# Kernel tuning notes

Measured on AMD Instinct MI355X. Metric: run time of the kernel, lower is better.

The kernel has to match this reference:

```python
import jax, jax.numpy as jnp
import numpy as np
from jax.scipy.special import gammaln

N_NODES = 50000
N_EDGES = 500000
IN_DIM = 256
OUT_DIM = 128
NEG_SLOPE = 0.01  # F.leaky_relu default


def setup_inputs() -> dict:
    key = jax.random.key(0)
    kh, kw, ka, ks, kd, kdist = jax.random.split(key, 6)
    h = jax.random.normal(kh, (N_NODES, IN_DIM), dtype=jnp.float32)
    # xavier-normal-ish scale for the learned weights
    fc_w = jax.random.normal(kw, (OUT_DIM, IN_DIM), dtype=jnp.float32) * 0.05
    attn_w = jax.random.normal(ka, (1, 2 * OUT_DIM), dtype=jnp.float32) * 0.05
    src = jax.random.randint(ks, (N_EDGES,), 0, N_NODES, dtype=jnp.int32)
    dst = jax.random.randint(kd, (N_EDGES,), 0, N_NODES, dtype=jnp.int32)
    dist = jax.random.randint(kdist, (N_EDGES,), 0, 100, dtype=jnp.int32)
    return {"h": h, "fc_w": fc_w, "attn_w": attn_w, "src": src, "dst": dst, "dist": dist}


def _poisson_pmf(k, mu):
    # poisson.pmf(k, mu) = exp(k*log(mu) - mu - lgamma(k+1))
    return jnp.exp(k * jnp.log(mu) - mu - gammaln(k + 1.0))


def reference(h, fc_w, attn_w, src, dst, dist):
    # node transform: z = fc(h), [N, out]
    z = h @ fc_w.T
    zs = z[src]            # [E, out] gathered source feats
    zd = z[dst]            # [E, out] gathered dest feats
    # attn_fc(cat([z_src, z_dst])) split into two dots
    a = zs @ attn_w[0, :OUT_DIM] + zd @ attn_w[0, OUT_DIM:]   # [E]
    e = jnp.where(a >= 0, a, NEG_SLOPE * a)                    # leaky_relu
    # poisson weighting: k = dist // 2, mu = mean(dists)
    dist_f = dist.astype(jnp.float32)
    mu = jnp.mean(dist_f)
    k = jnp.floor(dist_f / 2.0)
    probs = _poisson_pmf(k, mu)
    e = probs * e                                              # [E]
    # segment softmax over incoming edges of each dst node
    m = jax.ops.segment_max(e, dst, num_segments=N_NODES)      # [N]
    ex = jnp.exp(e - m[dst])                                   # [E]
    denom = jax.ops.segment_sum(ex, dst, num_segments=N_NODES) # [N]
    alpha = ex / denom[dst]                                    # [E]
    # weighted scatter-sum of source feats
    h_out = jax.ops.segment_sum(alpha[:, None] * zs, dst, num_segments=N_NODES)
    return h_out
```

## Files before the change

### kernel.cpp

```cpp
#include <hip/hip_runtime.h>
#include <math.h>

#define N_NODES 50000
#define N_EDGES 500000
#define IN_DIM 256
#define OUT_DIM 128
#define NEG_SLOPE 0.01f
#define NB_ZERO 196
#define MAX_DEG 128

typedef __attribute__((ext_vector_type(8))) short short8;
typedef __attribute__((ext_vector_type(4))) float f32x4;

__device__ __forceinline__ unsigned short f2bf(float f) {
  unsigned u = __float_as_uint(f);
  unsigned r = (u + 0x7FFFu + ((u >> 16) & 1u)) >> 16;
  return (unsigned short)r;
}
__device__ __forceinline__ float bflo(unsigned u) {
  return __uint_as_float((u & 0xFFFFu) << 16);
}
__device__ __forceinline__ float bfhi(unsigned u) {
  return __uint_as_float(u & 0xFFFF0000u);
}

__global__ __launch_bounds__(256) void prep_kernel(
    const float* __restrict__ W, unsigned short* __restrict__ Wb,
    int* __restrict__ p) {
  const int i = blockIdx.x * 256 + threadIdx.x;
  if (i < N_NODES + 1) p[i] = 0;
  if (i < IN_DIM * OUT_DIM) Wb[i] = f2bf(W[i]);
}

__global__ __launch_bounds__(512, 4) void gemm_mfma_kernel(
    const float* __restrict__ h, const unsigned short* __restrict__ Wb,
    const float* __restrict__ aw,
    unsigned short* __restrict__ zb, float* __restrict__ s1, float* __restrict__ s2) {
  __shared__ unsigned short Blds[128 * 256];
  const int t    = threadIdx.x;
  const int wid  = t >> 6;
  const int lane = t & 63;
  const int row0 = blockIdx.x * 128 + wid * 16;
  const int r16  = lane & 15;
  const int kg   = lane >> 4;

#pragma unroll
  for (int it = 0; it < 8; ++it) {
    const int c   = it * 512 + t;
    const int row = c >> 5, kc = c & 31;
    *(float4*)&Blds[row * 256 + ((kc ^ (row & 7)) << 3)] =
        *(const float4*)&Wb[row * 256 + (kc << 3)];
  }

  const int arow = row0 + r16;
  const size_t hbase = (size_t)((arow < N_NODES) ? arow : (N_NODES - 1)) * IN_DIM;
  float4 a0[8], a1[8];
#pragma unroll
  for (int ks = 0; ks < 8; ++ks) {
    const int k0 = ks * 32 + kg * 8;
    a0[ks] = *(const float4*)&h[hbase + k0];
    a1[ks] = *(const float4*)&h[hbase + k0 + 4];
  }

  f32x4 acc[8];
#pragma unroll
  for (int ct = 0; ct < 8; ++ct) acc[ct] = (f32x4)(0.f);

  __syncthreads();

#pragma unroll
  for (int ks = 0; ks < 8; ++ks) {
    const int k0 = ks * 32 + kg * 8;
    short8 af;
    af[0] = (short)f2bf(a0[ks].x); af[1] = (short)f2bf(a0[ks].y);
    af[2] = (short)f2bf(a0[ks].z); af[3] = (short)f2bf(a0[ks].w);
    af[4] = (short)f2bf(a1[ks].x); af[5] = (short)f2bf(a1[ks].y);
    af[6] = (short)f2bf(a1[ks].z); af[7] = (short)f2bf(a1[ks].w);
#pragma unroll
    for (int ct = 0; ct < 8; ++ct) {
      const int brow = ct * 16 + r16;
      const short8 bf =
          *(const short8*)&Blds[brow * 256 + (k0 ^ ((r16 & 7) << 3))];
      acc[ct] = __builtin_amdgcn_mfma_f32_16x16x32_bf16(af, bf, acc[ct], 0, 0, 0);
    }
  }

#pragma unroll
  for (int q = 0; q < 4; ++q) {
    const int zr = row0 + kg * 4 + q;
    if (zr < N_NODES) {
#pragma unroll
      for (int ct = 0; ct < 8; ++ct)
        zb[(size_t)zr * OUT_DIM + ct * 16 + r16] = f2bf(acc[ct][q]);
    }
  }

  float p1[4] = {0.f, 0.f, 0.f, 0.f}, p2[4] = {0.f, 0.f, 0.f, 0.f};
#pragma unroll
  for (int ct = 0; ct < 8; ++ct) {
    const float w1 = aw[ct * 16 + r16];
    const float w2 = aw[128 + ct * 16 + r16];
#pragma unroll
    for (int q = 0; q < 4; ++q) {
      p1[q] += acc[ct][q] * w1;
      p2[q] += acc[ct][q] * w2;
    }
  }
#pragma unroll
  for (int off = 8; off; off >>= 1) {
#pragma unroll
    for (int q = 0; q < 4; ++q) {
      p1[q] += __shfl_xor(p1[q], off);
      p2[q] += __shfl_xor(p2[q], off);
    }
  }
  if (r16 == 0) {
#pragma unroll
    for (int q = 0; q < 4; ++q) {
      const int zr = row0 + kg * 4 + q;
      if (zr < N_NODES) { s1[zr] = p1[q]; s2[zr] = p2[q]; }
    }
  }
}

__global__ __launch_bounds__(256) void mean_hist_kernel(
    const int* __restrict__ dist, const int* __restrict__ dst,
    int* __restrict__ isum, int* __restrict__ cnt, int* __restrict__ rank) {
  int tid = blockIdx.x * blockDim.x + threadIdx.x;
  int stride = gridDim.x * blockDim.x;
  int acc = 0;
  for (int i = tid; i < N_EDGES; i += stride) {
    acc += dist[i];
    rank[i] = atomicAdd(&cnt[dst[i]], 1);
  }
#pragma unroll
  for (int off = 32; off; off >>= 1) acc += __shfl_down(acc, off);
  if ((threadIdx.x & 63) == 0) atomicAdd(isum, acc);
}

__global__ __launch_bounds__(128) void lut_kernel(
    const int* __restrict__ isum, float* __restrict__ lut) {
  const int d = threadIdx.x;
  if (d >= 100) return;
  const float mu = (float)(*isum) * (1.0f / N_EDGES);
  const float k = (float)(d >> 1);
  lut[d] = expf(k * logf(mu) - mu - lgammaf(k + 1.0f));
}

__global__ __launch_bounds__(256) void fill_kernel(
    const int* __restrict__ dst, const int* __restrict__ src,
    const int* __restrict__ dist, const int* __restrict__ rank,
    const float* __restrict__ s1, const float* __restrict__ s2,
    const float* __restrict__ lut, float2* __restrict__ epair) {
  int i = blockIdx.x * blockDim.x + threadIdx.x;
  if (i >= N_EDGES) return;
  const int d = dst[i];
  const int s = src[i];
  const int r = rank[i];
  if (r >= MAX_DEG) return;
  const float p = lut[dist[i]];
  const float a = s1[s] + s2[d];
  const float ev = p * ((a >= 0.f) ? a : NEG_SLOPE * a);
  epair[(size_t)d * MAX_DEG + r] = make_float2(expf(ev), __int_as_float(s));
}

__global__ __launch_bounds__(256) void node_kernel(
    const int* __restrict__ cnt, const float2* __restrict__ epair,
    const uint4* __restrict__ zb4, float* __restrict__ out) {
  const int wid = threadIdx.x >> 6, lane = threadIdx.x & 63;
  const int n = blockIdx.x * 4 + wid;
  if (n >= N_NODES) return;
  const size_t beg = (size_t)n * MAX_DEG;
  const int deg = min(cnt[n], MAX_DEG);

  const int q     = lane >> 4;
  const int laneQ = lane & 15;

  float acc[8] = {0.f, 0.f, 0.f, 0.f, 0.f, 0.f, 0.f, 0.f};
  if (deg > 0) {
    float ss = 0.f;
    for (int j = lane; j < deg; j += 64) ss += epair[beg + j].x;
#pragma unroll
    for (int off = 32; off; off >>= 1) ss += __shfl_xor(ss, off);
    const float inv = 1.0f / ss;

#pragma unroll 2
    for (int jj = 0; jj < deg; jj += 4) {
      int j2 = jj + q;
      const float w = (j2 < deg) ? 1.0f : 0.0f;
      j2 = (j2 < deg) ? j2 : jj;
      const float2 pr = epair[beg + j2];
      const float al = pr.x * inv * w;
      const int   sj = __float_as_int(pr.y);
      const uint4 v = zb4[(size_t)sj * 16 + laneQ];
      acc[0] += al * bflo(v.x); acc[1] += al * bfhi(v.x);
      acc[2] += al * bflo(v.y); acc[3] += al * bfhi(v.y);
      acc[4] += al * bflo(v.z); acc[5] += al * bfhi(v.z);
      acc[6] += al * bflo(v.w); acc[7] += al * bfhi(v.w);
    }
  }

#pragma unroll
  for (int k = 0; k < 8; ++k) {
    acc[k] += __shfl_down(acc[k], 16);
    acc[k] += __shfl_down(acc[k], 32);
  }
  if (lane < 16) {
    float* orow = &out[(size_t)n * OUT_DIM + laneQ * 8];
    *(float4*)&orow[0] = make_float4(acc[0], acc[1], acc[2], acc[3]);
    *(float4*)&orow[4] = make_float4(acc[4], acc[5], acc[6], acc[7]);
  }
}

extern "C" void kernel_launch(void* const* d_in, const int* in_sizes, int n_in,
                              void* d_out, int out_size, void* d_ws, size_t ws_size,
                              hipStream_t stream) {
  const float* h    = (const float*)d_in[0];
  const float* fc_w = (const float*)d_in[1];
  const float* attn = (const float*)d_in[2];
  const int*   src  = (const int*)d_in[3];
  const int*   dst  = (const int*)d_in[4];
  const int*   dist = (const int*)d_in[5];
  float* out = (float*)d_out;
  float* ws  = (float*)d_ws;

  unsigned short* zb    = (unsigned short*)ws;
  float*          s1    = ws + 3200000;
  float*          s2    = ws + 3250000;
  int*            cnt   = (int*)(ws + 3300000);
  int*            isum  = (int*)(ws + 3350000);
  float*          lut   = ws + 3350004;
  int*            rank  = (int*)(ws + 3350104);
  float2*         epair = (float2*)(ws + 3850104);
  unsigned short* Wb    = (unsigned short*)(ws + 16650104);

  prep_kernel<<<NB_ZERO, 256, 0, stream>>>(fc_w, Wb, cnt);
  gemm_mfma_kernel<<<(N_NODES + 127) / 128, 512, 0, stream>>>(h, Wb, attn, zb, s1, s2);
  mean_hist_kernel<<<256, 256, 0, stream>>>(dist, dst, isum, cnt, rank);
  lut_kernel<<<1, 128, 0, stream>>>(isum, lut);
  fill_kernel<<<(N_EDGES + 255) / 256, 256, 0, stream>>>(
      dst, src, dist, rank, s1, s2, lut, epair);
  node_kernel<<<(N_NODES + 3) / 4, 256, 0, stream>>>(
      cnt, epair, (const uint4*)zb, out);
}
```

Baseline: 94.83 us.

## Fuse edge scoring into node kernel and pack src/dist slots during histogram

The histogram kernel now writes each edge's src index and dist, packed into 32 bits, straight into its per-destination slot, which removes the rank array. The separate fill kernel is gone. The node kernel computes the leaky-relu attention, Poisson weight and exp per edge itself and stages weight/index pairs in shared memory. This cuts one launch and the 8-byte epair write and read, at the cost of random s1 reads inside the node kernel. The packing relies on src < 65536 and dist < 65536, and the grid uses N_NODES/4, which assumes N_NODES is divisible by 4.

```diff
diff --git a/kernel.cpp b/kernel.cpp
--- a/kernel.cpp
+++ b/kernel.cpp
@@ -125,13 +125,18 @@
 
 __global__ __launch_bounds__(256) void mean_hist_kernel(
     const int* __restrict__ dist, const int* __restrict__ dst,
-    int* __restrict__ isum, int* __restrict__ cnt, int* __restrict__ rank) {
+    const int* __restrict__ src,
+    int* __restrict__ isum, int* __restrict__ cnt, unsigned* __restrict__ slots) {
   int tid = blockIdx.x * blockDim.x + threadIdx.x;
   int stride = gridDim.x * blockDim.x;
   int acc = 0;
   for (int i = tid; i < N_EDGES; i += stride) {
-    acc += dist[i];
-    rank[i] = atomicAdd(&cnt[dst[i]], 1);
+    const int dd = dist[i];
+    const int d  = dst[i];
+    acc += dd;
+    const int r = atomicAdd(&cnt[d], 1);
+    if (r < MAX_DEG)
+      slots[(size_t)d * MAX_DEG + r] = (unsigned)src[i] | ((unsigned)dd << 16);
   }
 #pragma unroll
   for (int off = 32; off; off >>= 1) acc += __shfl_down(acc, off);
@@ -147,29 +152,14 @@
   lut[d] = expf(k * logf(mu) - mu - lgammaf(k + 1.0f));
 }
 
-__global__ __launch_bounds__(256) void fill_kernel(
-    const int* __restrict__ dst, const int* __restrict__ src,
-    const int* __restrict__ dist, const int* __restrict__ rank,
+__global__ __launch_bounds__(256) void node_kernel(
+    const int* __restrict__ cnt, const unsigned* __restrict__ slots,
     const float* __restrict__ s1, const float* __restrict__ s2,
-    const float* __restrict__ lut, float2* __restrict__ epair) {
-  int i = blockIdx.x * blockDim.x + threadIdx.x;
-  if (i >= N_EDGES) return;
-  const int d = dst[i];
-  const int s = src[i];
-  const int r = rank[i];
-  if (r >= MAX_DEG) return;
-  const float p = lut[dist[i]];
-  const float a = s1[s] + s2[d];
-  const float ev = p * ((a >= 0.f) ? a : NEG_SLOPE * a);
-  epair[(size_t)d * MAX_DEG + r] = make_float2(expf(ev), __int_as_float(s));
-}
-
-__global__ __launch_bounds__(256) void node_kernel(
-    const int* __restrict__ cnt, const float2* __restrict__ epair,
+    const float* __restrict__ lut,
     const uint4* __restrict__ zb4, float* __restrict__ out) {
+  __shared__ uint2 pl[4][MAX_DEG];
   const int wid = threadIdx.x >> 6, lane = threadIdx.x & 63;
   const int n = blockIdx.x * 4 + wid;
-  if (n >= N_NODES) return;
   const size_t beg = (size_t)n * MAX_DEG;
   const int deg = min(cnt[n], MAX_DEG);
 
@@ -178,8 +168,17 @@
 
   float acc[8] = {0.f, 0.f, 0.f, 0.f, 0.f, 0.f, 0.f, 0.f};
   if (deg > 0) {
+    const float s2n = s2[n];
     float ss = 0.f;
-    for (int j = lane; j < deg; j += 64) ss += epair[beg + j].x;
+    for (int j = lane; j < deg; j += 64) {
+      const unsigned pk = slots[beg + j];
+      const unsigned sidx = pk & 0xFFFFu;
+      const float a = s1[sidx] + s2n;
+      const float lr = (a >= 0.f) ? a : NEG_SLOPE * a;
+      const float xe = expf(lut[pk >> 16] * lr);
+      pl[wid][j] = make_uint2(__float_as_uint(xe), sidx);
+      ss += xe;
+    }
 #pragma unroll
     for (int off = 32; off; off >>= 1) ss += __shfl_xor(ss, off);
     const float inv = 1.0f / ss;
@@ -189,10 +188,9 @@
       int j2 = jj + q;
       const float w = (j2 < deg) ? 1.0f : 0.0f;
       j2 = (j2 < deg) ? j2 : jj;
-      const float2 pr = epair[beg + j2];
-      const float al = pr.x * inv * w;
-      const int   sj = __float_as_int(pr.y);
-      const uint4 v = zb4[(size_t)sj * 16 + laneQ];
+      const uint2 pr = pl[wid][j2];
+      const float al = __uint_as_float(pr.x) * inv * w;
+      const uint4 v = zb4[(size_t)pr.y * 16 + laneQ];
       acc[0] += al * bflo(v.x); acc[1] += al * bfhi(v.x);
       acc[2] += al * bflo(v.y); acc[3] += al * bfhi(v.y);
       acc[4] += al * bflo(v.z); acc[5] += al * bfhi(v.z);
@@ -230,16 +228,13 @@
   int*            cnt   = (int*)(ws + 3300000);
   int*            isum  = (int*)(ws + 3350000);
   float*          lut   = ws + 3350004;
-  int*            rank  = (int*)(ws + 3350104);
-  float2*         epair = (float2*)(ws + 3850104);
-  unsigned short* Wb    = (unsigned short*)(ws + 16650104);
+  unsigned*       slots = (unsigned*)(ws + 3350104);
+  unsigned short* Wb    = (unsigned short*)(ws + 9750104);
 
   prep_kernel<<<NB_ZERO, 256, 0, stream>>>(fc_w, Wb, cnt);
   gemm_mfma_kernel<<<(N_NODES + 127) / 128, 512, 0, stream>>>(h, Wb, attn, zb, s1, s2);
-  mean_hist_kernel<<<256, 256, 0, stream>>>(dist, dst, isum, cnt, rank);
+  mean_hist_kernel<<<256, 256, 0, stream>>>(dist, dst, src, isum, cnt, slots);
   lut_kernel<<<1, 128, 0, stream>>>(isum, lut);
-  fill_kernel<<<(N_EDGES + 255) / 256, 256, 0, stream>>>(
-      dst, src, dist, rank, s1, s2, lut, epair);
-  node_kernel<<<(N_NODES + 3) / 4, 256, 0, stream>>>(
-      cnt, epair, (const uint4*)zb, out);
-}
+  node_kernel<<<N_NODES / 4, 256, 0, stream>>>(
+      cnt, slots, s1, s2, lut, (const uint4*)zb, out);
+}
```

Result: faster. 88.80 us (-6.4%).
